# Kernel optimization log

Hardware: AMD Instinct MI355X
Metric: run time of the kernel (lower is better)

## Reference

```python
import jax, jax.numpy as jnp
import numpy as np
import math

B, S, H, NH, HD = 2, 2048, 4096, 32, 128  # batch, seq, hidden, heads, head_dim
ROPE_BASE = 10000.0


def setup_inputs() -> dict:
    key = jax.random.key(0)
    k1, k2 = jax.random.split(key)
    hidden_states = jax.random.normal(k1, (B, S, H), jnp.float32) * 0.02
    W_pack = jax.random.normal(k2, (3 * H, H), jnp.float32) * (1.0 / math.sqrt(H))
    position_ids = jnp.tile(jnp.arange(S, dtype=jnp.int64)[None, :], (B, 1))
    # 4D additive causal mask, as passed by HF Baichuan to this attention module
    causal = jnp.triu(jnp.full((S, S), -1e9, jnp.float32), 1)[None, None, :, :]
    return {"hidden_states": hidden_states, "W_pack": W_pack,
            "attention_mask": causal, "position_ids": position_ids}


def _rope(x, position_ids):
    # x: [B, S, NH, HD]; NeoX-style rotate-half RoPE over full head_dim
    half = HD // 2
    inv_freq = 1.0 / (ROPE_BASE ** (jnp.arange(half, dtype=jnp.float32) / half))
    ang = position_ids.astype(jnp.float32)[:, :, None] * inv_freq  # [B,S,half]
    cos = jnp.concatenate([jnp.cos(ang), jnp.cos(ang)], axis=-1)[:, :, None, :]
    sin = jnp.concatenate([jnp.sin(ang), jnp.sin(ang)], axis=-1)[:, :, None, :]
    x1, x2 = jnp.split(x, 2, axis=-1)
    x_rot = jnp.concatenate([-x2, x1], axis=-1)
    return x * cos + x_rot * sin


def reference(hidden_states, W_pack, attention_mask, position_ids):
    # fused QKV projection (W_pack has no bias in Baichuan)
    proj = hidden_states @ W_pack.T                      # [B,S,3H]
    q, k, v = jnp.split(proj, 3, axis=-1)
    q = q.reshape(B, S, NH, HD)
    k = k.reshape(B, S, NH, HD)
    v = v.reshape(B, S, NH, HD)
    q = _rope(q, position_ids)
    k = _rope(k, position_ids)
    # scaled dot-product attention
    scale = 1.0 / math.sqrt(HD)
    q = q.transpose(0, 2, 1, 3)  # [B,NH,S,HD]
    k = k.transpose(0, 2, 1, 3)
    v = v.transpose(0, 2, 1, 3)
    scores = jnp.einsum("bhqd,bhkd->bhqk", q, k) * scale + attention_mask
    probs = jax.nn.softmax(scores, axis=-1)
    ctx = jnp.einsum("bhqk,bhkd->bhqd", probs, v)        # [B,NH,S,HD]
    attn_output = ctx.transpose(0, 2, 1, 3).reshape(B, S, H)
    return attn_output
```

## Files before the change

kernel.cpp:

```cpp
#include <hip/hip_runtime.h>
#include <hip/hip_bf16.h>
#include <stdint.h>

typedef unsigned short u16;
typedef __attribute__((ext_vector_type(8))) short s16x8;
typedef __attribute__((ext_vector_type(8))) unsigned short u16x8;
typedef __attribute__((ext_vector_type(4))) unsigned short u16x4;
typedef __attribute__((ext_vector_type(4))) float fx4;
typedef __bf16 bf16x8 __attribute__((ext_vector_type(8)));

#define SEQ 2048
#define HID 4096
#define NHEAD 32
#define HDIM 128
#define P3H 12288
#define NKT 64

__device__ __forceinline__ u16 f2bf(float f) {
  unsigned u = __builtin_bit_cast(unsigned, f);
  u += 0x7fffu + ((u >> 16) & 1u);
  return (u16)(u >> 16);
}
__device__ __forceinline__ float bf2f(u16 h) {
  unsigned u = ((unsigned)h) << 16;
  return __builtin_bit_cast(float, u);
}
__device__ __forceinline__ void gload_lds16(const void* g, void* l) {
  __builtin_amdgcn_global_load_lds((const __attribute__((address_space(1))) void*)g,
                                   (__attribute__((address_space(3))) void*)l, 16, 0, 0);
}
__device__ __forceinline__ fx4 mfma16(s16x8 a, s16x8 b, fx4 c) {
  return __builtin_amdgcn_mfma_f32_16x16x32_bf16(
      __builtin_bit_cast(bf16x8, a), __builtin_bit_cast(bf16x8, b), c, 0, 0, 0);
}

__global__ void k_cvt2(const float* __restrict__ s0, u16* __restrict__ d0, int n0,
                       const float* __restrict__ s1, u16* __restrict__ d1, int n1) {
  int i = blockIdx.x * blockDim.x + threadIdx.x;
  const float* src; u16* dst;
  if (i < n0) { src = s0; dst = d0; }
  else        { src = s1; dst = d1; i -= n0; if (i >= n1) return; }
  float4 v = reinterpret_cast<const float4*>(src)[i];
  u16x4 o;
  o[0] = f2bf(v.x); o[1] = f2bf(v.y); o[2] = f2bf(v.z); o[3] = f2bf(v.w);
  reinterpret_cast<u16x4*>(dst)[i] = o;
}

__device__ __forceinline__ void stage_half(const u16* __restrict__ g, u16* l, int r0, int t) {
#pragma unroll
  for (int c = 0; c < 2; c++) {
    int row = r0 + c * 64 + (t >> 3);
    int blk = (t & 7) ^ ((t >> 3) & 7);
    gload_lds16(g + (size_t)row * HID + blk * 8, l + row * 64 + (t & 7) * 8);
  }
}

#define BAR_OPEN __builtin_amdgcn_s_barrier()
#define BAR_CLOSE do { __builtin_amdgcn_s_barrier(); __builtin_amdgcn_sched_barrier(0); } while (0)
#define LGKM0 do { asm volatile("s_waitcnt lgkmcnt(0)" ::: "memory"); \
                   __builtin_amdgcn_sched_barrier(0); } while (0)

#define LDA_QUAD(qm) do { \
  _Pragma("unroll") for (int mi = 0; mi < 4; mi++) \
  _Pragma("unroll") for (int ks = 0; ks < 2; ks++) { \
    int row = wrr + (qm) * 64 + mi * 16 + li; \
    aA[mi][ks] = *(const s16x8*)&Al[row * 64 + (((ks * 4 + lg) ^ (row & 7)) << 3)]; \
  } } while (0)

#define LDB_QUAD(qn) do { \
  _Pragma("unroll") for (int nn = 0; nn < 2; nn++) \
  _Pragma("unroll") for (int ks = 0; ks < 2; ks++) { \
    int row = hh2 * 128 + qq2 * 32 + (qn) * 64 + nn * 16 + li; \
    aB[qn][nn][ks] = *(const s16x8*)&Bl[row * 64 + (((ks * 4 + lg) ^ (row & 7)) << 3)]; \
  } } while (0)

#define MMA_QUAD(qm, qn) do { \
  _Pragma("unroll") for (int ks = 0; ks < 2; ks++) \
  _Pragma("unroll") for (int mi = 0; mi < 4; mi++) \
  _Pragma("unroll") for (int ni = 0; ni < 2; ni++) \
    acc[(qm) * 4 + mi][(qn) * 2 + ni] = \
        mfma16(aA[mi][ks], aB[qn][ni][ks], acc[(qm) * 4 + mi][(qn) * 2 + ni]); \
  } while (0)

#define LTIDX(c, r) (((c) << 8) + ((r) ^ (((c) & 31) << 3)))

__global__ void __launch_bounds__(512, 2) k_gemm_qkv(const u16* __restrict__ A,
                                                     const u16* __restrict__ W,
                                                     u16* __restrict__ qo,
                                                     u16* __restrict__ ko,
                                                     u16* __restrict__ vo,
                                                     const int* __restrict__ pos) {
  __shared__ u16 SM[2][2][256 * 64];
  const int t = threadIdx.x;
  const int lane = t & 63;
  const int w = t >> 6;
  const int li = lane & 15, lg = lane >> 4;
  const int wr = w >> 2, wc = w & 3;
  const int wrr = wr * 128;
  const int hh2 = wc >> 1, qq2 = wc & 1;

  const int cpx = gridDim.x >> 3;
  const int swz = (blockIdx.x & 7) * cpx + (blockIdx.x >> 3);
  const int bm = swz / 48, bn = swz - bm * 48;
  const int m0 = bm * 256, n0 = bn * 256;

  const u16* Ag = A + (size_t)m0 * HID;
  const u16* Wg = W + (size_t)n0 * HID;

  fx4 acc[8][4];
#pragma unroll
  for (int i = 0; i < 8; i++)
#pragma unroll
    for (int j = 0; j < 4; j++) acc[i][j] = fx4{0.f, 0.f, 0.f, 0.f};
  s16x8 aA[4][2], aB[2][2][2];

  stage_half(Wg, &SM[0][1][0], 0, t);
  stage_half(Wg, &SM[0][1][0], 128, t);
  stage_half(Ag, &SM[0][0][0], 0, t);
  stage_half(Ag, &SM[0][0][0], 128, t);
  stage_half(Wg + 64, &SM[1][1][0], 0, t);
  stage_half(Wg + 64, &SM[1][1][0], 128, t);
  asm volatile("s_waitcnt vmcnt(4)" ::: "memory");
  BAR_CLOSE;

  for (int kt = 0; kt < NKT; kt++) {
    const int cur = kt & 1;
    u16* Al = &SM[cur][0][0];
    u16* Bl = &SM[cur][1][0];
    u16* Anxt = &SM[cur ^ 1][0][0];
    const u16* Agn = Ag + (size_t)(kt + 1) * 64;
    const u16* Wgn = Wg + (size_t)(kt + 2) * 64;

    LDA_QUAD(0);
    LDB_QUAD(0);
    if (kt + 1 < NKT) stage_half(Agn, Anxt, 0, t);
    asm volatile("s_waitcnt lgkmcnt(8)" ::: "memory");
    BAR_OPEN;
    LGKM0;
    __builtin_amdgcn_s_setprio(1);
    MMA_QUAD(0, 0);
    __builtin_amdgcn_s_setprio(0);
    BAR_CLOSE;

    LDB_QUAD(1);
    if (kt + 1 < NKT) stage_half(Agn, Anxt, 128, t);
    BAR_OPEN;
    LGKM0;
    __builtin_amdgcn_s_setprio(1);
    MMA_QUAD(0, 1);
    __builtin_amdgcn_s_setprio(0);
    BAR_CLOSE;

    LDA_QUAD(1);
    if (kt + 2 < NKT) stage_half(Wgn, Bl, 0, t);
    BAR_OPEN;
    LGKM0;
    __builtin_amdgcn_s_setprio(1);
    MMA_QUAD(1, 1);
    __builtin_amdgcn_s_setprio(0);
    BAR_CLOSE;

    if (kt + 2 < NKT) stage_half(Wgn, Bl, 128, t);
    BAR_OPEN;
    LGKM0;
    __builtin_amdgcn_s_setprio(1);
    MMA_QUAD(1, 0);
    __builtin_amdgcn_s_setprio(0);
    if (kt + 2 < NKT) {
      asm volatile("s_waitcnt vmcnt(4)" ::: "memory");
    } else {
      asm volatile("s_waitcnt vmcnt(0)" ::: "memory");
    }
    BAR_CLOSE;
  }

  const int ttype = n0 >> 12;
  const int h0 = (n0 & 4095) >> 7;
  const int bb = m0 >> 11;
  const int sB = m0 & 2047;

  if (ttype < 2) {
    u16* dst = (ttype == 0) ? qo : ko;
    const float LG2E4 = 0.2076205059304601f;
    const float LG2_2PI = 2.6514961294723187f;
#pragma unroll
    for (int p = 0; p < 2; p++) {
      int d = qq2 * 32 + p * 16 + li;
      float invf2 = exp2f(__builtin_fmaf(-(float)d, LG2E4, -LG2_2PI));
#pragma unroll
      for (int mi = 0; mi < 8; mi++) {
        int r0 = wrr + mi * 16 + lg * 4;
        int4 p4 = *reinterpret_cast<const int4*>(&pos[m0 + r0]);
#pragma unroll
        for (int j = 0; j < 4; j++) {
          float pv = (float)((j == 0) ? p4.x : (j == 1) ? p4.y : (j == 2) ? p4.z : p4.w);
          float rev = pv * invf2;
          rev -= floorf(rev);
          float sn = __builtin_amdgcn_sinf(rev);
          float cs = __builtin_amdgcn_cosf(rev);
          float x1 = acc[mi][p][j], x2 = acc[mi][p + 2][j];
          size_t base = ((size_t)(bb * NHEAD + h0 + hh2) * SEQ + sB + r0 + j) * HDIM;
          dst[base + d]      = f2bf(x1 * cs - x2 * sn);
          dst[base + d + 64] = f2bf(x2 * cs + x1 * sn);
        }
      }
    }
  } else {
    u16* LT = &SM[0][0][0];
#pragma unroll
    for (int mi = 0; mi < 8; mi++)
#pragma unroll
      for (int c2 = 0; c2 < 4; c2++) {
        u16x4 pk;
#pragma unroll
        for (int j = 0; j < 4; j++) pk[j] = f2bf(acc[mi][c2][j]);
        int c = hh2 * 128 + qq2 * 32 + (c2 >> 1) * 64 + (c2 & 1) * 16 + li;
        int r0 = wrr + mi * 16 + lg * 4;
        *reinterpret_cast<u16x4*>(&LT[LTIDX(c, r0)]) = pk;
      }
    __syncthreads();
    for (int it = 0; it < 16; ++it) {
      int cp = w * 16 + it;
      int c = cp * 2 + (lane >> 5);
      int ch = lane & 31;
      u16x8 v = *reinterpret_cast<const u16x8*>(&LT[LTIDX(c, ch * 8)]);
      int hh = c >> 7, d = c & 127;
      size_t base = ((size_t)(bb * NHEAD + h0 + hh) * HDIM + d) * SEQ + sB;
      *reinterpret_cast<u16x8*>(&vo[base + ch * 8]) = v;
    }
  }
}

__device__ __forceinline__ void stage_kv(const u16* __restrict__ kp, const u16* __restrict__ vp,
                                         u16* ksl, u16* vsl, int kv0, int t) {
#pragma unroll
  for (int c = 0; c < 4; c++) {
    int row = c * 16 + (t >> 4);
    int cb = (t & 15) ^ (row & 7);
    gload_lds16(kp + (size_t)(kv0 + row) * HDIM + cb * 8, ksl + (size_t)(c * 256 + t) * 8);
  }
#pragma unroll
  for (int c = 0; c < 4; c++) {
    int row = c * 32 + (t >> 3);
    int cb = (t & 7) ^ (row & 7);
    gload_lds16(vp + (size_t)row * SEQ + kv0 + cb * 8, vsl + (size_t)(c * 256 + t) * 8);
  }
}

__global__ void __launch_bounds__(256, 2) k_attn(const u16* __restrict__ q,
                                                 const u16* __restrict__ k,
                                                 const u16* __restrict__ vt,
                                                 float* __restrict__ out) {
  __shared__ u16 Ks[2][64 * 128];
  __shared__ u16 Vs[2][128 * 64];
  __shared__ u16 Ps[4][2][16 * 64];
  const int t = threadIdx.x;
  const int w = t >> 6, lane = t & 63;
  const int li = lane & 15, lg = lane >> 4;
  const int bh = blockIdx.x;
  const int qb = gridDim.y - 1 - blockIdx.y;
  const int b = bh >> 5, h = bh & 31;
  const int qw = qb * 128 + w * 32;
  const u16* qp = q + (size_t)bh * SEQ * HDIM;
  const u16* kp = k + (size_t)bh * SEQ * HDIM;
  const u16* vp = vt + (size_t)bh * HDIM * SEQ;

  s16x8 bq[2][4];
#pragma unroll
  for (int g = 0; g < 2; g++)
#pragma unroll
    for (int kk = 0; kk < 4; kk++)
      bq[g][kk] = *reinterpret_cast<const s16x8*>(
          &qp[(size_t)(qw + g * 16 + li) * HDIM + kk * 32 + lg * 8]);

  fx4 Oacc[2][8];
#pragma unroll
  for (int g = 0; g < 2; g++)
#pragma unroll
    for (int nd = 0; nd < 8; nd++) Oacc[g][nd] = fx4{0.f, 0.f, 0.f, 0.f};
  float mrun[2] = {-1e30f, -1e30f}, lrun[2] = {0.f, 0.f};

  const float SC2 = 0.12752551286084110f;
  const float THR = 8.0f / SC2;
  const int nt = 2 * (qb + 1);
  const int psw = (li & 7) << 4;

  stage_kv(kp, vp, Ks[0], Vs[0], 0, t);

  for (int tk = 0; tk < nt; tk++) {
    const int cur = tk & 1;
    if (tk + 1 < nt) {
      stage_kv(kp, vp, Ks[cur ^ 1], Vs[cur ^ 1], (tk + 1) * 64, t);
      asm volatile("s_waitcnt vmcnt(8)" ::: "memory");
    } else {
      asm volatile("s_waitcnt vmcnt(0)" ::: "memory");
    }
    __builtin_amdgcn_s_barrier();

    const u16* Kc = Ks[cur];
    const u16* Vc = Vs[cur];
    const int kv0 = tk * 64;
    const bool diag = (tk >= 2 * qb);

    fx4 sc[2][4];
#pragma unroll
    for (int g = 0; g < 2; g++)
#pragma unroll
      for (int n = 0; n < 4; n++) sc[g][n] = fx4{0.f, 0.f, 0.f, 0.f};
    __builtin_amdgcn_s_setprio(1);
#pragma unroll
    for (int n = 0; n < 4; n++) {
      int r = n * 16 + li;
#pragma unroll
      for (int kk = 0; kk < 4; kk++) {
        s16x8 ak = *reinterpret_cast<const s16x8*>(
            &Kc[r * 128 + (((kk * 4 + lg) ^ (r & 7)) << 3)]);
        sc[0][n] = mfma16(ak, bq[0][kk], sc[0][n]);
        sc[1][n] = mfma16(ak, bq[1][kk], sc[1][n]);
      }
    }
    __builtin_amdgcn_s_setprio(0);

    if (diag) {
#pragma unroll
      for (int g = 0; g < 2; g++) {
        const int qg = qw + g * 16 + li;
#pragma unroll
        for (int n = 0; n < 4; n++)
#pragma unroll
          for (int j = 0; j < 4; j++) {
            int kvg = kv0 + n * 16 + lg * 4 + j;
            if (kvg > qg) sc[g][n][j] = -1e30f;
          }
      }
    }

    s16x8 ap[2][2];
#pragma unroll
    for (int g = 0; g < 2; g++) {
      float mn[4];
#pragma unroll
      for (int n = 0; n < 4; n++)
        mn[n] = fmaxf(fmaxf(sc[g][n][0], sc[g][n][1]), fmaxf(sc[g][n][2], sc[g][n][3]));
      float vmax = fmaxf(fmaxf(mn[0], mn[1]), fmaxf(mn[2], mn[3]));
      vmax = fmaxf(vmax, __shfl_xor(vmax, 16));
      vmax = fmaxf(vmax, __shfl_xor(vmax, 32));
      if (__any(vmax > mrun[g] + THR)) {
        float mnew = fmaxf(mrun[g], vmax);
        float al = exp2f((mrun[g] - mnew) * SC2);
        mrun[g] = mnew;
        lrun[g] *= al;
        float alj[4];
#pragma unroll
        for (int j = 0; j < 4; j++) alj[j] = __shfl(al, lg * 4 + j);
#pragma unroll
        for (int nd = 0; nd < 8; nd++)
#pragma unroll
          for (int j = 0; j < 4; j++) Oacc[g][nd][j] *= alj[j];
      }
      const float mS = mrun[g] * SC2;
      float ps[4];
#pragma unroll
      for (int n = 0; n < 4; n++) {
        u16x4 pk;
        float pv0 = exp2f(__builtin_fmaf(sc[g][n][0], SC2, -mS));
        float pv1 = exp2f(__builtin_fmaf(sc[g][n][1], SC2, -mS));
        float pv2 = exp2f(__builtin_fmaf(sc[g][n][2], SC2, -mS));
        float pv3 = exp2f(__builtin_fmaf(sc[g][n][3], SC2, -mS));
        pk[0] = __builtin_bit_cast(u16, __float2bfloat16(pv0));
        pk[1] = __builtin_bit_cast(u16, __float2bfloat16(pv1));
        pk[2] = __builtin_bit_cast(u16, __float2bfloat16(pv2));
        pk[3] = __builtin_bit_cast(u16, __float2bfloat16(pv3));
        ps[n] = (pv0 + pv1) + (pv2 + pv3);
        *reinterpret_cast<u16x4*>(
            &Ps[w][g][li * 64 + (((n * 32 + lg * 8) ^ psw) >> 1)]) = pk;
      }
      float psum = (ps[0] + ps[1]) + (ps[2] + ps[3]);
      psum += __shfl_xor(psum, 16);
      psum += __shfl_xor(psum, 32);
      lrun[g] += psum;
#pragma unroll
      for (int kvc = 0; kvc < 2; kvc++)
        ap[g][kvc] = *reinterpret_cast<const s16x8*>(
            &Ps[w][g][li * 64 + (((kvc * 64 + lg * 16) ^ psw) >> 1)]);
    }

    __builtin_amdgcn_s_setprio(1);
#pragma unroll
    for (int nd = 0; nd < 8; nd++) {
      int dr = nd * 16 + li;
#pragma unroll
      for (int kvc = 0; kvc < 2; kvc++) {
        s16x8 bv = *reinterpret_cast<const s16x8*>(
            &Vc[dr * 64 + (((kvc * 4 + lg) ^ (dr & 7)) << 3)]);
        Oacc[0][nd] = mfma16(ap[0][kvc], bv, Oacc[0][nd]);
        Oacc[1][nd] = mfma16(ap[1][kvc], bv, Oacc[1][nd]);
      }
    }
    __builtin_amdgcn_s_setprio(0);

    __builtin_amdgcn_s_barrier();
    __builtin_amdgcn_sched_barrier(0);
  }

#pragma unroll
  for (int g = 0; g < 2; g++)
#pragma unroll
    for (int j = 0; j < 4; j++) {
      float rl = 1.0f / __shfl(lrun[g], lg * 4 + j);
      int s = qw + g * 16 + lg * 4 + j;
      float* op = out + ((size_t)(b * SEQ) + s) * HID + h * HDIM;
#pragma unroll
      for (int nd = 0; nd < 8; nd++) op[nd * 16 + li] = Oacc[g][nd][j] * rl;
    }
}

extern "C" void kernel_launch(void* const* d_in, const int* in_sizes, int n_in,
                              void* d_out, int out_size, void* d_ws, size_t ws_size,
                              hipStream_t stream) {
  const float* hidden = (const float*)d_in[0];
  const float* wpack = (const float*)d_in[1];
  const int* pos = (const int*)d_in[3];
  float* out = (float*)d_out;

  char* ws = (char*)d_ws;
  u16* hid_bf = (u16*)ws;
  u16* wp_bf = (u16*)(ws + ((size_t)32 << 20));
  u16* qb = (u16*)(ws + ((size_t)128 << 20));
  u16* kb = (u16*)(ws + ((size_t)160 << 20));
  u16* vtb = (u16*)(ws + ((size_t)192 << 20));

  const int n4h = HID * HID / 4, n4w = P3H * HID / 4;
  k_cvt2<<<(n4h + n4w + 255) / 256, 256, 0, stream>>>(hidden, hid_bf, n4h, wpack, wp_bf, n4w);

  k_gemm_qkv<<<768, 512, 0, stream>>>(hid_bf, wp_bf, qb, kb, vtb, pos);

  dim3 ga(2 * NHEAD, SEQ / 128);
  k_attn<<<ga, 256, 0, stream>>>(qb, kb, vtb, out);
}
```

Baseline: 533.0 us.

## Enlarge attention query tile to 256 rows with 8 waves; unroll GEMM k-loop by two

The attention kernel now runs 512-thread blocks covering 256 query rows, so each staged K/V tile is shared by eight waves instead of four. This halves K/V global traffic per query row, but it halves the grid, coarsens the causal load balance, and drops the occupancy hint to one block per CU. Separately, the QKV GEMM k-loop is manually unrolled by two so the double-buffer index becomes a compile-time constant.

```diff
diff --git a/kernel.cpp b/kernel.cpp
--- a/kernel.cpp
+++ b/kernel.cpp
@@ -81,6 +81,57 @@
     acc[(qm) * 4 + mi][(qn) * 2 + ni] = \
         mfma16(aA[mi][ks], aB[qn][ni][ks], acc[(qm) * 4 + mi][(qn) * 2 + ni]); \
   } while (0)
+
+#define KTILE_BODY(ktv, cur) do { \
+  const int kt = (ktv); \
+  u16* Al = &SM[cur][0][0]; \
+  u16* Bl = &SM[cur][1][0]; \
+  u16* Anxt = &SM[(cur) ^ 1][0][0]; \
+  const u16* Agn = Ag + (size_t)(kt + 1) * 64; \
+  const u16* Wgn = Wg + (size_t)(kt + 2) * 64; \
+   \
+  LDA_QUAD(0); \
+  LDB_QUAD(0); \
+  if (kt + 1 < NKT) stage_half(Agn, Anxt, 0, t); \
+  asm volatile("s_waitcnt lgkmcnt(8)" ::: "memory"); \
+  BAR_OPEN; \
+  LGKM0; \
+  __builtin_amdgcn_s_setprio(1); \
+  MMA_QUAD(0, 0); \
+  __builtin_amdgcn_s_setprio(0); \
+  BAR_CLOSE; \
+   \
+  LDB_QUAD(1); \
+  if (kt + 1 < NKT) stage_half(Agn, Anxt, 128, t); \
+  BAR_OPEN; \
+  LGKM0; \
+  __builtin_amdgcn_s_setprio(1); \
+  MMA_QUAD(0, 1); \
+  __builtin_amdgcn_s_setprio(0); \
+  BAR_CLOSE; \
+   \
+  LDA_QUAD(1); \
+  if (kt + 2 < NKT) stage_half(Wgn, Bl, 0, t); \
+  BAR_OPEN; \
+  LGKM0; \
+  __builtin_amdgcn_s_setprio(1); \
+  MMA_QUAD(1, 1); \
+  __builtin_amdgcn_s_setprio(0); \
+  BAR_CLOSE; \
+   \
+  if (kt + 2 < NKT) stage_half(Wgn, Bl, 128, t); \
+  BAR_OPEN; \
+  LGKM0; \
+  __builtin_amdgcn_s_setprio(1); \
+  MMA_QUAD(1, 0); \
+  __builtin_amdgcn_s_setprio(0); \
+  if (kt + 2 < NKT) { \
+    asm volatile("s_waitcnt vmcnt(4)" ::: "memory"); \
+  } else { \
+    asm volatile("s_waitcnt vmcnt(0)" ::: "memory"); \
+  } \
+  BAR_CLOSE; \
+} while (0)
 
 #define LTIDX(c, r) (((c) << 8) + ((r) ^ (((c) & 31) << 3)))
 
@@ -123,55 +174,9 @@
   asm volatile("s_waitcnt vmcnt(4)" ::: "memory");
   BAR_CLOSE;
 
-  for (int kt = 0; kt < NKT; kt++) {
-    const int cur = kt & 1;
-    u16* Al = &SM[cur][0][0];
-    u16* Bl = &SM[cur][1][0];
-    u16* Anxt = &SM[cur ^ 1][0][0];
-    const u16* Agn = Ag + (size_t)(kt + 1) * 64;
-    const u16* Wgn = Wg + (size_t)(kt + 2) * 64;
-
-    LDA_QUAD(0);
-    LDB_QUAD(0);
-    if (kt + 1 < NKT) stage_half(Agn, Anxt, 0, t);
-    asm volatile("s_waitcnt lgkmcnt(8)" ::: "memory");
-    BAR_OPEN;
-    LGKM0;
-    __builtin_amdgcn_s_setprio(1);
-    MMA_QUAD(0, 0);
-    __builtin_amdgcn_s_setprio(0);
-    BAR_CLOSE;
-
-    LDB_QUAD(1);
-    if (kt + 1 < NKT) stage_half(Agn, Anxt, 128, t);
-    BAR_OPEN;
-    LGKM0;
-    __builtin_amdgcn_s_setprio(1);
-    MMA_QUAD(0, 1);
-    __builtin_amdgcn_s_setprio(0);
-    BAR_CLOSE;
-
-    LDA_QUAD(1);
-    if (kt + 2 < NKT) stage_half(Wgn, Bl, 0, t);
-    BAR_OPEN;
-    LGKM0;
-    __builtin_amdgcn_s_setprio(1);
-    MMA_QUAD(1, 1);
-    __builtin_amdgcn_s_setprio(0);
-    BAR_CLOSE;
-
-    if (kt + 2 < NKT) stage_half(Wgn, Bl, 128, t);
-    BAR_OPEN;
-    LGKM0;
-    __builtin_amdgcn_s_setprio(1);
-    MMA_QUAD(1, 0);
-    __builtin_amdgcn_s_setprio(0);
-    if (kt + 2 < NKT) {
-      asm volatile("s_waitcnt vmcnt(4)" ::: "memory");
-    } else {
-      asm volatile("s_waitcnt vmcnt(0)" ::: "memory");
-    }
-    BAR_CLOSE;
+  for (int kt2 = 0; kt2 < NKT; kt2 += 2) {
+    KTILE_BODY(kt2, 0);
+    KTILE_BODY(kt2 + 1, 1);
   }
 
   const int ttype = n0 >> 12;
@@ -234,33 +239,33 @@
 __device__ __forceinline__ void stage_kv(const u16* __restrict__ kp, const u16* __restrict__ vp,
                                          u16* ksl, u16* vsl, int kv0, int t) {
 #pragma unroll
-  for (int c = 0; c < 4; c++) {
-    int row = c * 16 + (t >> 4);
+  for (int c = 0; c < 2; c++) {
+    int row = c * 32 + (t >> 4);
     int cb = (t & 15) ^ (row & 7);
-    gload_lds16(kp + (size_t)(kv0 + row) * HDIM + cb * 8, ksl + (size_t)(c * 256 + t) * 8);
-  }
-#pragma unroll
-  for (int c = 0; c < 4; c++) {
-    int row = c * 32 + (t >> 3);
+    gload_lds16(kp + (size_t)(kv0 + row) * HDIM + cb * 8, ksl + (size_t)(c * 512 + t) * 8);
+  }
+#pragma unroll
+  for (int c = 0; c < 2; c++) {
+    int row = c * 64 + (t >> 3);
     int cb = (t & 7) ^ (row & 7);
-    gload_lds16(vp + (size_t)row * SEQ + kv0 + cb * 8, vsl + (size_t)(c * 256 + t) * 8);
-  }
-}
-
-__global__ void __launch_bounds__(256, 2) k_attn(const u16* __restrict__ q,
+    gload_lds16(vp + (size_t)row * SEQ + kv0 + cb * 8, vsl + (size_t)(c * 512 + t) * 8);
+  }
+}
+
+__global__ void __launch_bounds__(512, 1) k_attn(const u16* __restrict__ q,
                                                  const u16* __restrict__ k,
                                                  const u16* __restrict__ vt,
                                                  float* __restrict__ out) {
   __shared__ u16 Ks[2][64 * 128];
   __shared__ u16 Vs[2][128 * 64];
-  __shared__ u16 Ps[4][2][16 * 64];
+  __shared__ u16 Ps[8][2][16 * 64];
   const int t = threadIdx.x;
   const int w = t >> 6, lane = t & 63;
   const int li = lane & 15, lg = lane >> 4;
   const int bh = blockIdx.x;
   const int qb = gridDim.y - 1 - blockIdx.y;
   const int b = bh >> 5, h = bh & 31;
-  const int qw = qb * 128 + w * 32;
+  const int qw = qb * 256 + w * 32;
   const u16* qp = q + (size_t)bh * SEQ * HDIM;
   const u16* kp = k + (size_t)bh * SEQ * HDIM;
   const u16* vp = vt + (size_t)bh * HDIM * SEQ;
@@ -282,7 +287,7 @@
 
   const float SC2 = 0.12752551286084110f;
   const float THR = 8.0f / SC2;
-  const int nt = 2 * (qb + 1);
+  const int nt = 4 * (qb + 1);
   const int psw = (li & 7) << 4;
 
   stage_kv(kp, vp, Ks[0], Vs[0], 0, t);
@@ -291,7 +296,7 @@
     const int cur = tk & 1;
     if (tk + 1 < nt) {
       stage_kv(kp, vp, Ks[cur ^ 1], Vs[cur ^ 1], (tk + 1) * 64, t);
-      asm volatile("s_waitcnt vmcnt(8)" ::: "memory");
+      asm volatile("s_waitcnt vmcnt(4)" ::: "memory");
     } else {
       asm volatile("s_waitcnt vmcnt(0)" ::: "memory");
     }
@@ -300,7 +305,7 @@
     const u16* Kc = Ks[cur];
     const u16* Vc = Vs[cur];
     const int kv0 = tk * 64;
-    const bool diag = (tk >= 2 * qb);
+    const bool diag = (tk >= 4 * qb);
 
     fx4 sc[2][4];
 #pragma unroll
@@ -435,6 +440,6 @@
 
   k_gemm_qkv<<<768, 512, 0, stream>>>(hid_bf, wp_bf, qb, kb, vtb, pos);
 
-  dim3 ga(2 * NHEAD, SEQ / 128);
-  k_attn<<<ga, 256, 0, stream>>>(qb, kb, vtb, out);
-}
+  dim3 ga(2 * NHEAD, SEQ / 256);
+  k_attn<<<ga, 512, 0, stream>>>(qb, kb, vtb, out);
+}
```

After: 539.1 us. Within noise of the previous version (+1.1%).
